# Kernel optimization log

Hardware: AMD Instinct MI355X
Metric: run time of the kernel (lower is better)

The kernel has to match this reference:

```python
import jax, jax.numpy as jnp
import numpy as np

NUM_HEAD = 12
DIM_MODEL = 768
HEAD_DIM = DIM_MODEL // NUM_HEAD


def setup_inputs() -> dict:
    key = jax.random.key(0)
    ks = jax.random.split(key, 4)
    B, S, D = 2, 2048, DIM_MODEL
    scale = 1.0 / np.sqrt(D)
    return {
        "v1": jax.random.normal(ks[0], (B, S, D), dtype=jnp.float32),
        "v1_mask": jnp.zeros((B, 1, 1, S), dtype=jnp.float32),
        "Wq": jax.random.normal(ks[1], (D, D), dtype=jnp.float32) * scale,
        "bq": jnp.zeros((D,), dtype=jnp.float32),
        "Wk": jax.random.normal(ks[2], (D, D), dtype=jnp.float32) * scale,
        "bk": jnp.zeros((D,), dtype=jnp.float32),
        "Wv": jax.random.normal(ks[3], (D, D), dtype=jnp.float32) * scale,
        "bv": jnp.zeros((D,), dtype=jnp.float32),
    }


def reference(v1, v1_mask, Wq, bq, Wk, bk, Wv, bv):
    B, S, D = v1.shape
    H, hd = NUM_HEAD, HEAD_DIM

    def split_heads(x):  # [B,S,D] -> [B,H,S,hd]
        return x.reshape(B, S, H, hd).transpose(0, 2, 1, 3)

    q = split_heads(v1 @ Wq + bq)
    k = split_heads(v1 @ Wk + bk)
    v = split_heads(v1 @ Wv + bv)

    scores = jnp.einsum("bhqd,bhkd->bhqk", q, k) / jnp.sqrt(jnp.float32(hd))
    scores = scores + v1_mask  # additive mask broadcasts over heads/query
    probs = jax.nn.softmax(scores, axis=-1)
    # dropout is identity in eval/reference mode
    ctx = jnp.einsum("bhqk,bhkd->bhqd", probs, v)
    return ctx.transpose(0, 2, 1, 3).reshape(B, S, D)
```

## Files before the change

### kernel.cpp

```cpp
#include <hip/hip_runtime.h>
#include <math.h>

#define B_SZ 2
#define S_SZ 2048
#define D_SZ 768
#define NH   12
#define HD   64
#define BH_T (B_SZ * NH)
#define M_TOT (B_SZ * S_SZ)

using bfrag = __attribute__((ext_vector_type(8))) short;
using ffrag = __attribute__((ext_vector_type(4))) float;

__device__ __forceinline__ unsigned short f2bf(float f) {
    unsigned int u = __float_as_uint(f);
    u += 0x7fffu + ((u >> 16) & 1u);
    return (unsigned short)(u >> 16);
}
__device__ __forceinline__ unsigned short f2bf_fast(float f) {
    return (unsigned short)((__float_as_uint(f) + 0x8000u) >> 16);
}

__device__ __forceinline__ void async16(void* lds, const void* gp) {
    __builtin_amdgcn_global_load_lds(
        (const __attribute__((address_space(1))) unsigned int*)gp,
        (__attribute__((address_space(3))) unsigned int*)lds,
        16, 0, 0);
}

__global__ __launch_bounds__(256) void prep(
    const float* __restrict__ v1,
    const float* __restrict__ Wq, const float* __restrict__ Wk,
    const float* __restrict__ Wv,
    unsigned short* __restrict__ v1b, unsigned short* __restrict__ Wt) {
    __shared__ float tile[64][65];
    const int bx = blockIdx.x;
    const int t = threadIdx.x;
    if (bx < 3072) {
        int i = (bx * 256 + t) * 4;
        float4 v = *(const float4*)&v1[i];
        ushort4 o;
        o.x = f2bf(v.x); o.y = f2bf(v.y); o.z = f2bf(v.z); o.w = f2bf(v.w);
        *(ushort4*)&v1b[i] = o;
    } else {
        int r = bx - 3072;
        int z = r / 144;
        int rr = r % 144;
        int n0 = (rr % 12) * 64, k0 = (rr / 12) * 64;
        const float* W = (z == 0) ? Wq : (z == 1) ? Wk : Wv;
        unsigned short* dst = Wt + (size_t)z * D_SZ * D_SZ;
        #pragma unroll
        for (int i = 0; i < 16; ++i) {
            int flat = i * 256 + t;
            int rr2 = flat >> 6, c = flat & 63;
            tile[rr2][c] = W[(size_t)(k0 + rr2) * D_SZ + n0 + c];
        }
        __syncthreads();
        #pragma unroll
        for (int i = 0; i < 16; ++i) {
            int flat = i * 256 + t;
            int rr2 = flat >> 6, c = flat & 63;
            dst[(size_t)(n0 + rr2) * D_SZ + k0 + c] = f2bf(tile[c][rr2]);
        }
    }
}

#define CP_LD 136
#define CPV_LD 72

__global__ __launch_bounds__(256) void proj_gemm(
    const unsigned short* __restrict__ Ab,
    const unsigned short* __restrict__ Wt,
    const float* __restrict__ bq, const float* __restrict__ bk_,
    const float* __restrict__ bv_,
    unsigned short* __restrict__ Qb, unsigned short* __restrict__ Kb,
    unsigned short* __restrict__ Vtb) {
    const int z = blockIdx.z;
    const unsigned short* Bt = Wt + (size_t)z * D_SZ * D_SZ;
    const float* bias = (z == 0) ? bq : (z == 1) ? bk_ : bv_;

    __shared__ unsigned short smem[64 * 64 + 128 * 64];
    unsigned short* As = smem;
    unsigned short* Bs = smem + 64 * 64;

    const int t = threadIdx.x;
    const int lane = t & 63;
    const int w = t >> 6;
    const int wm = w & 1, wn = w >> 1;
    const int col = lane & 15;
    const int quad = lane >> 4;
    const int m0 = blockIdx.y * 64;
    const int n0 = blockIdx.x * 128;
    const int wbase = t & ~63;

    ffrag acc[2][4];
    #pragma unroll
    for (int i = 0; i < 2; ++i)
        #pragma unroll
        for (int j = 0; j < 4; ++j) { ffrag zf = {0.f, 0.f, 0.f, 0.f}; acc[i][j] = zf; }

    for (int k0 = 0; k0 < D_SZ; k0 += 64) {
        __syncthreads();
        #pragma unroll
        for (int i = 0; i < 2; ++i) {
            int c = i * 256 + t;
            int row = c >> 3;
            int gcol = ((c & 7) ^ (row & 7)) * 8;
            async16(&As[(size_t)(i * 256 + wbase) * 8],
                    &Ab[(size_t)(m0 + row) * D_SZ + k0 + gcol]);
        }
        #pragma unroll
        for (int i = 0; i < 4; ++i) {
            int c = i * 256 + t;
            int row = c >> 3;
            int gcol = ((c & 7) ^ (row & 7)) * 8;
            async16(&Bs[(size_t)(i * 256 + wbase) * 8],
                    &Bt[(size_t)(n0 + row) * D_SZ + k0 + gcol]);
        }
        __syncthreads();
        #pragma unroll
        for (int kk = 0; kk < 64; kk += 32) {
            const int cc = (kk >> 3) + quad;
            bfrag a[2], b[4];
            #pragma unroll
            for (int mi = 0; mi < 2; ++mi) {
                int row = wm * 32 + mi * 16 + col;
                a[mi] = *(const bfrag*)&As[row * 64 + ((cc ^ (row & 7)) * 8)];
            }
            #pragma unroll
            for (int ni = 0; ni < 4; ++ni) {
                int row = wn * 64 + ni * 16 + col;
                b[ni] = *(const bfrag*)&Bs[row * 64 + ((cc ^ (row & 7)) * 8)];
            }
            if (z == 2) {
                #pragma unroll
                for (int mi = 0; mi < 2; ++mi)
                    #pragma unroll
                    for (int ni = 0; ni < 4; ++ni)
                        acc[mi][ni] = __builtin_amdgcn_mfma_f32_16x16x32_bf16(
                            a[mi], b[ni], acc[mi][ni], 0, 0, 0);
            } else {
                #pragma unroll
                for (int mi = 0; mi < 2; ++mi)
                    #pragma unroll
                    for (int ni = 0; ni < 4; ++ni)
                        acc[mi][ni] = __builtin_amdgcn_mfma_f32_16x16x32_bf16(
                            b[ni], a[mi], acc[mi][ni], 0, 0, 0);
            }
        }
    }

    __syncthreads();

    if (z < 2) {
        const float sc = (z == 0) ? 0.125f : 1.0f;
        #pragma unroll
        for (int mi = 0; mi < 2; ++mi) {
            int m_local = wm * 32 + mi * 16 + col;
            #pragma unroll
            for (int ni = 0; ni < 4; ++ni) {
                int n_base = wn * 64 + ni * 16 + quad * 4;
                float4 b4 = *(const float4*)&bias[n0 + n_base];
                uint2 pk;
                pk.x = (unsigned)f2bf((acc[mi][ni][0] + b4.x) * sc) |
                       ((unsigned)f2bf((acc[mi][ni][1] + b4.y) * sc) << 16);
                pk.y = (unsigned)f2bf((acc[mi][ni][2] + b4.z) * sc) |
                       ((unsigned)f2bf((acc[mi][ni][3] + b4.w) * sc) << 16);
                *(uint2*)&smem[m_local * CP_LD + n_base] = pk;
            }
        }
        __syncthreads();
        unsigned short* Out = (z == 0) ? Qb : Kb;
        #pragma unroll
        for (int j = 0; j < 4; ++j) {
            int flat = j * 256 + t;
            int row = flat >> 4;
            int ch = flat & 15;
            uint4 vv = *(const uint4*)&smem[row * CP_LD + ch * 8];
            int m = m0 + row;
            int bb = m >> 11, s = m & 2047;
            int h = (n0 >> 6) + (ch >> 3);
            int d = (ch & 7) * 8;
            *(uint4*)&Out[((size_t)(bb * NH + h) * S_SZ + s) * HD + d] = vv;
        }
    } else {
        #pragma unroll
        for (int ni = 0; ni < 4; ++ni) {
            int n_local = wn * 64 + ni * 16 + col;
            float bvv = bias[n0 + n_local];
            #pragma unroll
            for (int mi = 0; mi < 2; ++mi) {
                int m_base = wm * 32 + mi * 16 + quad * 4;
                uint2 pk;
                pk.x = (unsigned)f2bf(acc[mi][ni][0] + bvv) |
                       ((unsigned)f2bf(acc[mi][ni][1] + bvv) << 16);
                pk.y = (unsigned)f2bf(acc[mi][ni][2] + bvv) |
                       ((unsigned)f2bf(acc[mi][ni][3] + bvv) << 16);
                *(uint2*)&smem[n_local * CPV_LD + m_base] = pk;
            }
        }
        __syncthreads();
        #pragma unroll
        for (int j = 0; j < 4; ++j) {
            int flat = j * 256 + t;
            int row = flat >> 3;
            int ch = flat & 7;
            uint4 vv = *(const uint4*)&smem[row * CPV_LD + ch * 8];
            int n = n0 + row;
            int h = n >> 6, d = n & 63;
            int m = m0 + ch * 8;
            int bb = m >> 11, s = m & 2047;
            *(uint4*)&Vtb[((size_t)(bb * NH + h) * HD + d) * S_SZ + s] = vv;
        }
    }
}

__global__ __launch_bounds__(512) void attn_mfma(
    const unsigned short* __restrict__ Qb, const unsigned short* __restrict__ Kb,
    const unsigned short* __restrict__ Vt, const float* __restrict__ mask,
    float* __restrict__ out) {
    __shared__ union {
        unsigned short stage[2][2][64 * 64];
        struct { float Of[64][68]; float ls1[64]; } ep;
    } u;
    __shared__ unsigned short Ps[8][16 * 64];
    __shared__ float ms[2][64];

    const int t = threadIdx.x;
    const int lane = t & 63;
    const int w = t >> 6;
    const int g = w >> 2;
    const int wq = w & 3;
    const int tg = t & 255;
    const int col = lane & 15;
    const int quad = lane >> 4;
    const int q0 = blockIdx.x * 64;
    const int bh = blockIdx.y;
    const int b = bh / NH, h = bh % NH;
    const int wbase = tg & ~63;

    const unsigned short* Qg = Qb + (size_t)bh * S_SZ * HD;
    const unsigned short* Kg = Kb + (size_t)bh * S_SZ * HD;
    const unsigned short* Vg = Vt + (size_t)bh * S_SZ * HD;
    const float* mrow = mask + (size_t)b * S_SZ;

    {
        int row = t >> 3;
        int gcol = ((t & 7) ^ (row & 7)) * 8;
        async16(&u.stage[0][0][(size_t)(t & ~63) * 8],
                &Qg[(size_t)(q0 + row) * HD + gcol]);
    }
    __syncthreads();
    const int arow = wq * 16 + col;
    bfrag aq[2];
    #pragma unroll
    for (int kk = 0; kk < 2; ++kk) {
        int cc = kk * 4 + quad;
        aq[kk] = *(const bfrag*)&u.stage[0][0][arow * 64 + ((cc ^ (arow & 7)) * 8)];
    }

    ffrag o[4];
    #pragma unroll
    for (int i = 0; i < 4; ++i) { ffrag zf = {0.f, 0.f, 0.f, 0.f}; o[i] = zf; }
    float lsum[4] = {0.f, 0.f, 0.f, 0.f};

    const int kbeg = g * (S_SZ / 2);
    for (int k0 = kbeg; k0 < kbeg + S_SZ / 2; k0 += 64) {
        __syncthreads();
        #pragma unroll
        for (int i = 0; i < 2; ++i) {
            int c = i * 256 + tg;
            int row = c >> 3;
            int gcol = ((c & 7) ^ (row & 7)) * 8;
            async16(&u.stage[0][g][(size_t)(i * 256 + wbase) * 8],
                    &Kg[(size_t)(k0 + row) * HD + gcol]);
            async16(&u.stage[1][g][(size_t)(i * 256 + wbase) * 8],
                    &Vg[(size_t)row * S_SZ + k0 + gcol]);
        }
        if (tg < 16) async16(&ms[g][0], &mrow[k0 + tg * 4]);
        __syncthreads();

        const unsigned short* Ks = u.stage[0][g];
        const unsigned short* Vs = u.stage[1][g];

        ffrag s[4];
        #pragma unroll
        for (int i = 0; i < 4; ++i) { ffrag zf = {0.f, 0.f, 0.f, 0.f}; s[i] = zf; }
        #pragma unroll
        for (int kk = 0; kk < 2; ++kk) {
            const int cc = kk * 4 + quad;
            #pragma unroll
            for (int ni = 0; ni < 4; ++ni) {
                int brow = ni * 16 + col;
                bfrag bk8 = *(const bfrag*)&Ks[brow * 64 + ((cc ^ (brow & 7)) * 8)];
                s[ni] = __builtin_amdgcn_mfma_f32_16x16x32_bf16(aq[kk], bk8, s[ni], 0, 0, 0);
            }
        }

        #pragma unroll
        for (int ni = 0; ni < 4; ++ni) {
            float mv = ms[g][ni * 16 + col];
            #pragma unroll
            for (int r = 0; r < 4; ++r) {
                float e = __expf(s[ni][r] + mv);
                s[ni][r] = e;
                lsum[r] += e;
            }
        }

        unsigned short* Pw = &Ps[w][0];
        #pragma unroll
        for (int ni = 0; ni < 4; ++ni) {
            #pragma unroll
            for (int r = 0; r < 4; ++r) {
                int prow = quad * 4 + r;
                int pcol = ni * 16 + col;
                Pw[prow * 64 + (((pcol >> 3) ^ (prow & 7)) * 8) + (pcol & 7)] =
                    f2bf_fast(s[ni][r]);
            }
        }
        #pragma unroll
        for (int kk = 0; kk < 2; ++kk) {
            const int cc = kk * 4 + quad;
            bfrag ap = *(const bfrag*)&Pw[col * 64 + ((cc ^ (col & 7)) * 8)];
            #pragma unroll
            for (int di = 0; di < 4; ++di) {
                int vrow = di * 16 + col;
                bfrag bv8 = *(const bfrag*)&Vs[vrow * 64 + ((cc ^ (vrow & 7)) * 8)];
                o[di] = __builtin_amdgcn_mfma_f32_16x16x32_bf16(ap, bv8, o[di], 0, 0, 0);
            }
        }
    }

    #pragma unroll
    for (int r = 0; r < 4; ++r) {
        #pragma unroll
        for (int off = 1; off < 16; off <<= 1)
            lsum[r] += __shfl_xor(lsum[r], off);
    }

    __syncthreads();
    if (g == 1) {
        #pragma unroll
        for (int di = 0; di < 4; ++di) {
            int d = di * 16 + col;
            #pragma unroll
            for (int r = 0; r < 4; ++r)
                u.ep.Of[wq * 16 + quad * 4 + r][d] = o[di][r];
        }
        if (col == 0) {
            #pragma unroll
            for (int r = 0; r < 4; ++r)
                u.ep.ls1[wq * 16 + quad * 4 + r] = lsum[r];
        }
    }
    __syncthreads();
    if (g == 0) {
        float inv[4];
        #pragma unroll
        for (int r = 0; r < 4; ++r) {
            int qr = wq * 16 + quad * 4 + r;
            inv[r] = 1.0f / (lsum[r] + u.ep.ls1[qr]);
        }
        #pragma unroll
        for (int di = 0; di < 4; ++di) {
            int d = di * 16 + col;
            #pragma unroll
            for (int r = 0; r < 4; ++r) {
                int qr = wq * 16 + quad * 4 + r;
                out[((size_t)(b * S_SZ + q0 + qr)) * D_SZ + h * HD + d] =
                    (o[di][r] + u.ep.Of[qr][d]) * inv[r];
            }
        }
    }
}

extern "C" void kernel_launch(void* const* d_in, const int* in_sizes, int n_in,
                              void* d_out, int out_size, void* d_ws, size_t ws_size,
                              hipStream_t stream) {
    const float* v1   = (const float*)d_in[0];
    const float* mask = (const float*)d_in[1];
    const float* Wq   = (const float*)d_in[2];
    const float* bq   = (const float*)d_in[3];
    const float* Wk   = (const float*)d_in[4];
    const float* bk   = (const float*)d_in[5];
    const float* Wv   = (const float*)d_in[6];
    const float* bv   = (const float*)d_in[7];
    float* out = (float*)d_out;

    char* ws = (char*)d_ws;
    const size_t per_b = (size_t)BH_T * S_SZ * HD * 2;
    unsigned short* Qb  = (unsigned short*)(ws);
    unsigned short* Kb  = (unsigned short*)(ws + per_b);
    unsigned short* Vtb = (unsigned short*)(ws + 2 * per_b);
    unsigned short* v1b = (unsigned short*)(ws + 3 * per_b);
    unsigned short* Wt  = (unsigned short*)(ws + 3 * per_b + (size_t)M_TOT * D_SZ * 2);

    prep<<<dim3(3072 + 432), 256, 0, stream>>>(v1, Wq, Wk, Wv, v1b, Wt);
    proj_gemm<<<dim3(6, 64, 3), 256, 0, stream>>>(v1b, Wt, bq, bk, bv, Qb, Kb, Vtb);
    attn_mfma<<<dim3(32, 24), 512, 0, stream>>>(Qb, Kb, Vtb, mask, out);
}
```

Baseline: 160.2 us.

## Register-prefetch pipelining in GEMM and attention, drop split-K attention

Replaces the async global-to-LDS loads in the projection GEMM and the attention kernel with register prefetch of the next tile, issued after the LDS store barrier so global latency overlaps the MFMA work. The attention kernel no longer splits the key range across two 256-thread groups with an LDS reduction. It now uses 256-thread blocks processing 128-key tiles, with a remapped 1D grid that groups heads, and keeps the mask in registers. The trade is higher register pressure and half as many threads per query tile, in exchange for removing the split-K epilogue reduction and exposed load latency.

Result: slower. 279.9 us (+74.7%).

```diff
diff --git a/kernel.cpp b/kernel.cpp
--- a/kernel.cpp
+++ b/kernel.cpp
@@ -19,13 +19,6 @@
 }
 __device__ __forceinline__ unsigned short f2bf_fast(float f) {
     return (unsigned short)((__float_as_uint(f) + 0x8000u) >> 16);
-}
-
-__device__ __forceinline__ void async16(void* lds, const void* gp) {
-    __builtin_amdgcn_global_load_lds(
-        (const __attribute__((address_space(1))) unsigned int*)gp,
-        (__attribute__((address_space(3))) unsigned int*)lds,
-        16, 0, 0);
 }
 
 __global__ __launch_bounds__(256) void prep(
@@ -91,7 +84,23 @@
     const int quad = lane >> 4;
     const int m0 = blockIdx.y * 64;
     const int n0 = blockIdx.x * 128;
-    const int wbase = t & ~63;
+
+    const int ar0 = t >> 3,         ag0 = ((t & 7) ^ (ar0 & 7)) * 8;
+    const int ar1 = (256 + t) >> 3, ag1 = (((256 + t) & 7) ^ (ar1 & 7)) * 8;
+    int brr[4], bgg[4];
+    #pragma unroll
+    for (int i = 0; i < 4; ++i) {
+        int c = i * 256 + t;
+        brr[i] = c >> 3;
+        bgg[i] = ((c & 7) ^ (brr[i] & 7)) * 8;
+    }
+
+    uint4 areg0, areg1, breg[4];
+    areg0 = *(const uint4*)&Ab[(size_t)(m0 + ar0) * D_SZ + ag0];
+    areg1 = *(const uint4*)&Ab[(size_t)(m0 + ar1) * D_SZ + ag1];
+    #pragma unroll
+    for (int i = 0; i < 4; ++i)
+        breg[i] = *(const uint4*)&Bt[(size_t)(n0 + brr[i]) * D_SZ + bgg[i]];
 
     ffrag acc[2][4];
     #pragma unroll
@@ -101,23 +110,20 @@
 
     for (int k0 = 0; k0 < D_SZ; k0 += 64) {
         __syncthreads();
-        #pragma unroll
-        for (int i = 0; i < 2; ++i) {
-            int c = i * 256 + t;
-            int row = c >> 3;
-            int gcol = ((c & 7) ^ (row & 7)) * 8;
-            async16(&As[(size_t)(i * 256 + wbase) * 8],
-                    &Ab[(size_t)(m0 + row) * D_SZ + k0 + gcol]);
-        }
-        #pragma unroll
-        for (int i = 0; i < 4; ++i) {
-            int c = i * 256 + t;
-            int row = c >> 3;
-            int gcol = ((c & 7) ^ (row & 7)) * 8;
-            async16(&Bs[(size_t)(i * 256 + wbase) * 8],
-                    &Bt[(size_t)(n0 + row) * D_SZ + k0 + gcol]);
-        }
-        __syncthreads();
+        *(uint4*)&As[(size_t)t * 8] = areg0;
+        *(uint4*)&As[(size_t)(256 + t) * 8] = areg1;
+        #pragma unroll
+        for (int i = 0; i < 4; ++i)
+            *(uint4*)&Bs[(size_t)(i * 256 + t) * 8] = breg[i];
+        __syncthreads();
+        if (k0 + 64 < D_SZ) {
+            const int kn = k0 + 64;
+            areg0 = *(const uint4*)&Ab[(size_t)(m0 + ar0) * D_SZ + kn + ag0];
+            areg1 = *(const uint4*)&Ab[(size_t)(m0 + ar1) * D_SZ + kn + ag1];
+            #pragma unroll
+            for (int i = 0; i < 4; ++i)
+                breg[i] = *(const uint4*)&Bt[(size_t)(n0 + brr[i]) * D_SZ + kn + bgg[i]];
+        }
         #pragma unroll
         for (int kk = 0; kk < 64; kk += 32) {
             const int cc = (kk >> 3) + quad;
@@ -215,82 +221,89 @@
     }
 }
 
-__global__ __launch_bounds__(512) void attn_mfma(
+__global__ __launch_bounds__(256) void attn_mfma(
     const unsigned short* __restrict__ Qb, const unsigned short* __restrict__ Kb,
     const unsigned short* __restrict__ Vt, const float* __restrict__ mask,
     float* __restrict__ out) {
-    __shared__ union {
-        unsigned short stage[2][2][64 * 64];
-        struct { float Of[64][68]; float ls1[64]; } ep;
-    } u;
-    __shared__ unsigned short Ps[8][16 * 64];
-    __shared__ float ms[2][64];
+    __shared__ unsigned short Ks[128 * 64];
+    __shared__ unsigned short Vs[64 * 128];
+    __shared__ unsigned short Ps[4][16 * 64];
 
     const int t = threadIdx.x;
     const int lane = t & 63;
     const int w = t >> 6;
-    const int g = w >> 2;
-    const int wq = w & 3;
-    const int tg = t & 255;
     const int col = lane & 15;
     const int quad = lane >> 4;
-    const int q0 = blockIdx.x * 64;
-    const int bh = blockIdx.y;
+    const int id = blockIdx.x;
+    const int tt = id >> 3;
+    const int q0 = (tt & 31) * 64;
+    const int bh = (id & 7) + 8 * (tt >> 5);
     const int b = bh / NH, h = bh % NH;
-    const int wbase = tg & ~63;
 
     const unsigned short* Qg = Qb + (size_t)bh * S_SZ * HD;
     const unsigned short* Kg = Kb + (size_t)bh * S_SZ * HD;
     const unsigned short* Vg = Vt + (size_t)bh * S_SZ * HD;
     const float* mrow = mask + (size_t)b * S_SZ;
 
-    {
-        int row = t >> 3;
-        int gcol = ((t & 7) ^ (row & 7)) * 8;
-        async16(&u.stage[0][0][(size_t)(t & ~63) * 8],
-                &Qg[(size_t)(q0 + row) * HD + gcol]);
-    }
-    __syncthreads();
-    const int arow = wq * 16 + col;
+    const int arow = w * 16 + col;
     bfrag aq[2];
     #pragma unroll
-    for (int kk = 0; kk < 2; ++kk) {
-        int cc = kk * 4 + quad;
-        aq[kk] = *(const bfrag*)&u.stage[0][0][arow * 64 + ((cc ^ (arow & 7)) * 8)];
-    }
+    for (int kk = 0; kk < 2; ++kk)
+        aq[kk] = *(const bfrag*)&Qg[(size_t)(q0 + arow) * HD + (kk * 4 + quad) * 8];
+
+    int krw[4], kgc[4], vrw[4], vgc[4];
+    #pragma unroll
+    for (int i = 0; i < 4; ++i) {
+        int c = i * 256 + t;
+        krw[i] = c >> 3;
+        kgc[i] = ((c & 7) ^ (krw[i] & 7)) * 8;
+        vrw[i] = c >> 4;
+        int cp = c & 15;
+        vgc[i] = ((cp & 8) | ((cp ^ vrw[i]) & 7)) * 8;
+    }
+
+    uint4 kreg[4], vreg[4];
+    float mcur[8], mnext[8];
+    #pragma unroll
+    for (int i = 0; i < 4; ++i) {
+        kreg[i] = *(const uint4*)&Kg[(size_t)krw[i] * HD + kgc[i]];
+        vreg[i] = *(const uint4*)&Vg[(size_t)vrw[i] * S_SZ + vgc[i]];
+    }
+    #pragma unroll
+    for (int ni = 0; ni < 8; ++ni) mcur[ni] = mrow[ni * 16 + col];
 
     ffrag o[4];
     #pragma unroll
     for (int i = 0; i < 4; ++i) { ffrag zf = {0.f, 0.f, 0.f, 0.f}; o[i] = zf; }
     float lsum[4] = {0.f, 0.f, 0.f, 0.f};
 
-    const int kbeg = g * (S_SZ / 2);
-    for (int k0 = kbeg; k0 < kbeg + S_SZ / 2; k0 += 64) {
-        __syncthreads();
-        #pragma unroll
-        for (int i = 0; i < 2; ++i) {
-            int c = i * 256 + tg;
-            int row = c >> 3;
-            int gcol = ((c & 7) ^ (row & 7)) * 8;
-            async16(&u.stage[0][g][(size_t)(i * 256 + wbase) * 8],
-                    &Kg[(size_t)(k0 + row) * HD + gcol]);
-            async16(&u.stage[1][g][(size_t)(i * 256 + wbase) * 8],
-                    &Vg[(size_t)row * S_SZ + k0 + gcol]);
-        }
-        if (tg < 16) async16(&ms[g][0], &mrow[k0 + tg * 4]);
-        __syncthreads();
-
-        const unsigned short* Ks = u.stage[0][g];
-        const unsigned short* Vs = u.stage[1][g];
-
-        ffrag s[4];
-        #pragma unroll
-        for (int i = 0; i < 4; ++i) { ffrag zf = {0.f, 0.f, 0.f, 0.f}; s[i] = zf; }
+    for (int k0 = 0; k0 < S_SZ; k0 += 128) {
+        __syncthreads();
+        #pragma unroll
+        for (int i = 0; i < 4; ++i) {
+            *(uint4*)&Ks[(size_t)(i * 256 + t) * 8] = kreg[i];
+            *(uint4*)&Vs[(size_t)(i * 256 + t) * 8] = vreg[i];
+        }
+        __syncthreads();
+        if (k0 + 128 < S_SZ) {
+            const int kn = k0 + 128;
+            #pragma unroll
+            for (int i = 0; i < 4; ++i) {
+                kreg[i] = *(const uint4*)&Kg[(size_t)(kn + krw[i]) * HD + kgc[i]];
+                vreg[i] = *(const uint4*)&Vg[(size_t)vrw[i] * S_SZ + kn + vgc[i]];
+            }
+            #pragma unroll
+            for (int ni = 0; ni < 8; ++ni) mnext[ni] = mrow[kn + ni * 16 + col];
+        }
+
+        ffrag s[8];
+        #pragma unroll
+        for (int i = 0; i < 8; ++i) { ffrag zf = {0.f, 0.f, 0.f, 0.f}; s[i] = zf; }
         #pragma unroll
         for (int kk = 0; kk < 2; ++kk) {
             const int cc = kk * 4 + quad;
             #pragma unroll
-            for (int ni = 0; ni < 4; ++ni) {
+            for (int ni = 0; ni < 8; ++ni) {
                 int brow = ni * 16 + col;
                 bfrag bk8 = *(const bfrag*)&Ks[brow * 64 + ((cc ^ (brow & 7)) * 8)];
                 s[ni] = __builtin_amdgcn_mfma_f32_16x16x32_bf16(aq[kk], bk8, s[ni], 0, 0, 0);
@@ -298,11 +311,10 @@
         }
 
         #pragma unroll
-        for (int ni = 0; ni < 4; ++ni) {
-            float mv = ms[g][ni * 16 + col];
+        for (int ni = 0; ni < 8; ++ni) {
             #pragma unroll
             for (int r = 0; r < 4; ++r) {
-                float e = __expf(s[ni][r] + mv);
+                float e = __expf(s[ni][r] + mcur[ni]);
                 s[ni][r] = e;
                 lsum[r] += e;
             }
@@ -310,26 +322,34 @@
 
         unsigned short* Pw = &Ps[w][0];
         #pragma unroll
-        for (int ni = 0; ni < 4; ++ni) {
-            #pragma unroll
-            for (int r = 0; r < 4; ++r) {
-                int prow = quad * 4 + r;
-                int pcol = ni * 16 + col;
-                Pw[prow * 64 + (((pcol >> 3) ^ (prow & 7)) * 8) + (pcol & 7)] =
-                    f2bf_fast(s[ni][r]);
-            }
-        }
-        #pragma unroll
-        for (int kk = 0; kk < 2; ++kk) {
-            const int cc = kk * 4 + quad;
-            bfrag ap = *(const bfrag*)&Pw[col * 64 + ((cc ^ (col & 7)) * 8)];
-            #pragma unroll
-            for (int di = 0; di < 4; ++di) {
-                int vrow = di * 16 + col;
-                bfrag bv8 = *(const bfrag*)&Vs[vrow * 64 + ((cc ^ (vrow & 7)) * 8)];
-                o[di] = __builtin_amdgcn_mfma_f32_16x16x32_bf16(ap, bv8, o[di], 0, 0, 0);
-            }
-        }
+        for (int half = 0; half < 2; ++half) {
+            #pragma unroll
+            for (int ni = 0; ni < 4; ++ni) {
+                #pragma unroll
+                for (int r = 0; r < 4; ++r) {
+                    int prow = quad * 4 + r;
+                    int pcol = ni * 16 + col;
+                    Pw[prow * 64 + (((pcol >> 3) ^ (prow & 7)) * 8) + (pcol & 7)] =
+                        f2bf_fast(s[half * 4 + ni][r]);
+                }
+            }
+            #pragma unroll
+            for (int kk = 0; kk < 2; ++kk) {
+                const int cc = kk * 4 + quad;
+                bfrag ap = *(const bfrag*)&Pw[col * 64 + ((cc ^ (col & 7)) * 8)];
+                #pragma unroll
+                for (int di = 0; di < 4; ++di) {
+                    int vrow = di * 16 + col;
+                    int ch = half * 8 + kk * 4 + quad;
+                    bfrag bv8 = *(const bfrag*)
+                        &Vs[vrow * 128 + ((ch & 8) | ((ch ^ vrow) & 7)) * 8];
+                    o[di] = __builtin_amdgcn_mfma_f32_16x16x32_bf16(ap, bv8, o[di], 0, 0, 0);
+                }
+            }
+        }
+
+        #pragma unroll
+        for (int ni = 0; ni < 8; ++ni) mcur[ni] = mnext[ni];
     }
 
     #pragma unroll
@@ -338,39 +358,16 @@
         for (int off = 1; off < 16; off <<= 1)
             lsum[r] += __shfl_xor(lsum[r], off);
     }
-
-    __syncthreads();
-    if (g == 1) {
-        #pragma unroll
-        for (int di = 0; di < 4; ++di) {
-            int d = di * 16 + col;
-            #pragma unroll
-            for (int r = 0; r < 4; ++r)
-                u.ep.Of[wq * 16 + quad * 4 + r][d] = o[di][r];
-        }
-        if (col == 0) {
-            #pragma unroll
-            for (int r = 0; r < 4; ++r)
-                u.ep.ls1[wq * 16 + quad * 4 + r] = lsum[r];
-        }
-    }
-    __syncthreads();
-    if (g == 0) {
-        float inv[4];
+    float inv[4];
+    #pragma unroll
+    for (int r = 0; r < 4; ++r) inv[r] = 1.0f / lsum[r];
+    #pragma unroll
+    for (int di = 0; di < 4; ++di) {
+        int d = di * 16 + col;
         #pragma unroll
         for (int r = 0; r < 4; ++r) {
-            int qr = wq * 16 + quad * 4 + r;
-            inv[r] = 1.0f / (lsum[r] + u.ep.ls1[qr]);
-        }
-        #pragma unroll
-        for (int di = 0; di < 4; ++di) {
-            int d = di * 16 + col;
-            #pragma unroll
-            for (int r = 0; r < 4; ++r) {
-                int qr = wq * 16 + quad * 4 + r;
-                out[((size_t)(b * S_SZ + q0 + qr)) * D_SZ + h * HD + d] =
-                    (o[di][r] + u.ep.Of[qr][d]) * inv[r];
-            }
+            int q = q0 + w * 16 + quad * 4 + r;
+            out[((size_t)(b * S_SZ + q)) * D_SZ + h * HD + d] = o[di][r] * inv[r];
         }
     }
 }
@@ -398,5 +395,5 @@
 
     prep<<<dim3(3072 + 432), 256, 0, stream>>>(v1, Wq, Wk, Wv, v1b, Wt);
     proj_gemm<<<dim3(6, 64, 3), 256, 0, stream>>>(v1b, Wt, bq, bk, bv, Qb, Kb, Vtb);
-    attn_mfma<<<dim3(32, 24), 512, 0, stream>>>(Qb, Kb, Vtb, mask, out);
-}
+    attn_mfma<<<dim3(32 * 24), 256, 0, stream>>>(Qb, Kb, Vtb, mask, out);
+}
```
